# Kernel tuning notes

Hardware: AMD Instinct MI355X
Metric: run time of the kernel (lower is better)

## Reference

```python
import jax, jax.numpy as jnp
import numpy as np

N = 100000   # nodes
E = 1600000  # edges


def setup_inputs() -> dict:
    key = jax.random.key(0)
    ks = jax.random.split(key, 9)
    return {
        "in_feat": jax.random.normal(ks[0], (N, 256), jnp.float32),
        "W": jax.random.normal(ks[1], (256, 128), jnp.float32) * 0.05,
        "attn_l": jax.random.normal(ks[2], (1, 128), jnp.float32) * 0.1,
        "attn_r": jax.random.normal(ks[3], (1, 128), jnp.float32) * 0.1,
        "bias": jax.random.normal(ks[4], (1, 128), jnp.float32) * 0.01,
        "fc_w": jax.random.normal(ks[5], (128, 2), jnp.float32) * 0.1,
        "fc_b": jax.random.normal(ks[6], (2,), jnp.float32) * 0.01,
        "src": jax.random.randint(ks[7], (E,), 0, N, jnp.int32),
        "dst": jax.random.randint(ks[8], (E,), 0, N, jnp.int32),
    }


def reference(in_feat, W, attn_l, attn_r, bias, fc_w, fc_b, src, dst):
    # GATConv, num_heads=1 (head dim kept implicit since it is squeezed anyway)
    h = in_feat @ W                              # [N, F] projected features
    el = jnp.sum(h * attn_l, axis=-1)            # [N] left attention logits
    er = jnp.sum(h * attn_r, axis=-1)            # [N] right attention logits
    e = jax.nn.leaky_relu(el[src] + er[dst], negative_slope=0.2)  # [E]
    # edge softmax segmented by destination node (numerically stable)
    m = jax.ops.segment_max(e, dst, num_segments=N)               # [N]
    ex = jnp.exp(e - m[dst])                                      # [E]
    s = jax.ops.segment_sum(ex, dst, num_segments=N)              # [N]
    alpha = ex / jnp.where(s == 0, 1.0, s)[dst]                   # [E]
    # attention-weighted aggregation of source features to destinations
    agg = jax.ops.segment_sum(alpha[:, None] * h[src], dst, num_segments=N)  # [N, F]
    agg = agg + bias                                              # GATConv bias
    # head: ReLU -> Linear -> sigmoid
    out = jax.nn.sigmoid(jax.nn.relu(agg) @ fc_w + fc_b)          # [N, C]
    return out
```

## Files before the change

### kernel.cpp

```cpp
#include <hip/hip_runtime.h>
#include <cstdint>
#include <cstddef>

#define N_NODES 100000
#define E_EDGES 1600000
#define F_IN 256
#define F_OUT 128
#define NBKT 391
#define OBCAP 5120
#define GEMM_NB 1563
#define WCVT_NB 128

#define GLOBAL_AS __attribute__((address_space(1)))
#define LDS_AS    __attribute__((address_space(3)))

typedef __attribute__((ext_vector_type(8))) short  short8v;
typedef __attribute__((ext_vector_type(4))) float  float4v;

__device__ __forceinline__ unsigned short f2bf(float x) {
    union { float f; unsigned u; } v; v.f = x;
    unsigned r = v.u + 0x7fffu + ((v.u >> 16) & 1u);
    return (unsigned short)(r >> 16);
}

__device__ __forceinline__ unsigned cvt_pk_bf16(float lo, float hi) {
    unsigned r;
    asm("v_cvt_pk_bf16_f32 %0, %1, %2" : "=v"(r) : "v"(lo), "v"(hi));
    return r;
}

__global__ __launch_bounds__(256) void wcvt_hist(const float* __restrict__ W,
                                                 unsigned short* __restrict__ Wt,
                                                 const int* __restrict__ dst,
                                                 int* __restrict__ bcnt) {
    __shared__ int h[NBKT];
    int t = threadIdx.x;
    if (blockIdx.x < WCVT_NB) {
        int i = blockIdx.x * 256 + t;
        int k = i >> 7, j = i & 127;
        Wt[j * F_IN + k] = f2bf(W[i]);
        return;
    }
    int b = blockIdx.x - WCVT_NB;
    for (int i = t; i < NBKT; i += 256) h[i] = 0;
    __syncthreads();
    int e0  = b * 4096;
    int end = min(e0 + 4096, E_EDGES);
    for (int i = e0 + t; i < end; i += 256) atomicAdd(&h[dst[i] >> 8], 1);
    __syncthreads();
    for (int i = t; i < NBKT; i += 256) if (h[i]) atomicAdd(&bcnt[i], h[i]);
}

__global__ __launch_bounds__(512) void k_scan(const int* __restrict__ bcnt,
                                              int* __restrict__ bbase,
                                              int* __restrict__ bcur) {
    __shared__ int s[512];
    int t = threadIdx.x;
    int d = (t < NBKT) ? bcnt[t] : 0;
    s[t] = d;
    __syncthreads();
    for (int off = 1; off < 512; off <<= 1) {
        int v = (t >= off) ? s[t - off] : 0;
        __syncthreads();
        s[t] += v;
        __syncthreads();
    }
    if (t < NBKT) { int ex = s[t] - d; bbase[t] = ex; bcur[t] = ex; }
    if (t == NBKT - 1) bbase[NBKT] = s[t];
}

__global__ __launch_bounds__(256) void gemm_scatter(const float* __restrict__ A,
                                                    const unsigned short* __restrict__ Wt,
                                                    const float* __restrict__ attn_l,
                                                    const float* __restrict__ attn_r,
                                                    unsigned short* __restrict__ Hb,
                                                    float* __restrict__ el,
                                                    float* __restrict__ er,
                                                    const int* __restrict__ src,
                                                    const int* __restrict__ dst,
                                                    int* __restrict__ bcur,
                                                    unsigned int* __restrict__ epack) {
    __shared__ char smem[32 * 1024];
    int tid = threadIdx.x;

    if (blockIdx.x >= GEMM_NB) {
        int* h = (int*)smem;
        int b = blockIdx.x - GEMM_NB;
        for (int i = tid; i < NBKT; i += 256) h[i] = 0;
        __syncthreads();
        int e0  = b * 4096;
        int end = min(e0 + 4096, E_EDGES);
        #pragma unroll
        for (int j = 0; j < 16; ++j) {
            int i = e0 + j * 256 + tid;
            if (i < end) atomicAdd(&h[dst[i] >> 8], 1);
        }
        __syncthreads();
        for (int i = tid; i < NBKT; i += 256) {
            int c = h[i];
            h[i] = c ? atomicAdd(&bcur[i], c) : 0;
        }
        __syncthreads();
        #pragma unroll
        for (int j = 0; j < 16; ++j) {
            int i = e0 + j * 256 + tid;
            if (i < end) {
                int dv = dst[i];
                int p = atomicAdd(&h[dv >> 8], 1);
                epack[p] = (unsigned)src[i] | ((unsigned)(dv & 255) << 17);
            }
        }
        return;
    }

    float*          Afs = (float*)smem;
    unsigned short* Bs  = (unsigned short*)(smem + 16 * 1024);
    int wave = tid >> 6, lane = tid & 63;
    int g = lane >> 4, c = lane & 15;
    int row0 = blockIdx.x * 64;
    float4v acc[8] = {};

    int a_r[4], a_k[4], a_w[4];
    #pragma unroll
    for (int i = 0; i < 4; ++i) {
        int W_ = i * 1024 + tid * 4;
        int r  = W_ >> 6;
        a_w[i] = W_;
        a_r[i] = min(row0 + r, N_NODES - 1);
        a_k[i] = (W_ & 63) ^ ((r & 15) << 2);
    }
    int b_j[4], b_k[4], b_u[4];
    #pragma unroll
    for (int i = 0; i < 4; ++i) {
        int U_ = i * 2048 + tid * 8;
        int j  = U_ >> 6;
        b_u[i] = U_;
        b_j[i] = j;
        b_k[i] = (U_ & 63) ^ ((j & 7) << 3);
    }

    for (int k0 = 0; k0 < F_IN; k0 += 64) {
        #pragma unroll
        for (int i = 0; i < 4; ++i) {
            __builtin_amdgcn_global_load_lds(
                (const GLOBAL_AS unsigned int*)(A + (size_t)a_r[i] * F_IN + k0 + a_k[i]),
                (LDS_AS unsigned int*)&Afs[a_w[i]], 16, 0, 0);
        }
        #pragma unroll
        for (int i = 0; i < 4; ++i) {
            __builtin_amdgcn_global_load_lds(
                (const GLOBAL_AS unsigned int*)(Wt + (size_t)b_j[i] * F_IN + k0 + b_k[i]),
                (LDS_AS unsigned int*)&Bs[b_u[i]], 16, 0, 0);
        }
        __syncthreads();
        int arow = wave * 16 + c;
        int aswz = (arow & 15) << 2;
        #pragma unroll
        for (int ks = 0; ks < 2; ++ks) {
            int woff = arow * 64 + ks * 32 + g * 8;
            float4 a0 = *reinterpret_cast<float4*>(&Afs[(woff)     ^ aswz]);
            float4 a1 = *reinterpret_cast<float4*>(&Afs[(woff + 4) ^ aswz]);
            unsigned u[4];
            u[0] = cvt_pk_bf16(a0.x, a0.y);
            u[1] = cvt_pk_bf16(a0.z, a0.w);
            u[2] = cvt_pk_bf16(a1.x, a1.y);
            u[3] = cvt_pk_bf16(a1.z, a1.w);
            short8v af = *reinterpret_cast<short8v*>(u);
            #pragma unroll
            for (int nt = 0; nt < 8; ++nt) {
                int j = nt * 16 + c;
                int boff = (j * 64 + ks * 32 + g * 8) ^ ((j & 7) << 3);
                short8v bf = *reinterpret_cast<short8v*>(&Bs[boff]);
                acc[nt] = __builtin_amdgcn_mfma_f32_16x16x32_bf16(af, bf, acc[nt], 0, 0, 0);
            }
        }
        __syncthreads();
    }

    float al[8], ar[8];
    #pragma unroll
    for (int nt = 0; nt < 8; ++nt) {
        al[nt] = attn_l[nt * 16 + c];
        ar[nt] = attn_r[nt * 16 + c];
    }
    #pragma unroll
    for (int r = 0; r < 4; ++r) {
        int grow = row0 + wave * 16 + g * 4 + r;
        float sl = 0.f, sr = 0.f;
        #pragma unroll
        for (int nt = 0; nt < 8; ++nt) {
            float h = acc[nt][r];
            sl += h * al[nt];
            sr += h * ar[nt];
        }
        if (grow < N_NODES) {
            #pragma unroll
            for (int nt = 0; nt < 8; ++nt)
                Hb[(size_t)grow * F_OUT + nt * 16 + c] = f2bf(acc[nt][r]);
        }
        #pragma unroll
        for (int off = 1; off < 16; off <<= 1) {
            sl += __shfl_xor(sl, off);
            sr += __shfl_xor(sr, off);
        }
        if (c == 0 && grow < N_NODES) { el[grow] = sl; er[grow] = sr; }
    }
}

__global__ __launch_bounds__(256) void k_sort2(const unsigned int* __restrict__ epack,
                                               const int* __restrict__ bbase,
                                               const float* __restrict__ el,
                                               const float* __restrict__ er,
                                               float2* __restrict__ exs,
                                               int* __restrict__ rowptr,
                                               int* __restrict__ deg) {
    __shared__ int hist[256], cur[256], s[256];
    __shared__ float ssl[256];
    __shared__ unsigned obuf[OBCAP];
    __shared__ float exb[OBCAP];
    int b = blockIdx.x, t = threadIdx.x;
    int base = bbase[b], end = bbase[b + 1];
    int cnt  = end - base;
    hist[t] = 0;
    ssl[t] = 0.f;
    __syncthreads();
    for (int i = t; i < cnt; i += 256) atomicAdd(&hist[epack[base + i] >> 17], 1);
    __syncthreads();
    int d = hist[t];
    s[t] = d;
    __syncthreads();
    for (int off = 1; off < 256; off <<= 1) {
        int v = (t >= off) ? s[t - off] : 0;
        __syncthreads();
        s[t] += v;
        __syncthreads();
    }
    int excl = s[t] - d;
    int n = b * 256 + t;
    if (n < N_NODES) { deg[n] = d; rowptr[n] = base + excl; }
    cur[t] = excl;
    __syncthreads();
    for (int i = t; i < cnt; i += 256) {
        unsigned e = epack[base + i];
        int d2  = e >> 17;
        int sid = (int)(e & 0x1FFFFu);
        float tv = el[sid] + er[b * 256 + d2];
        tv = tv > 0.f ? tv : 0.2f * tv;
        float ex = __expf(tv);
        int p = atomicAdd(&cur[d2], 1);
        if (p < OBCAP) { obuf[p] = e; exb[p] = ex; }
        atomicAdd(&ssl[d2], ex);
    }
    __syncthreads();
    for (int i = t; i < cnt; i += 256) {
        unsigned e = obuf[i];
        float alpha = exb[i] / ssl[e >> 17];
        exs[base + i] = make_float2(alpha, __uint_as_float((e & 0x1FFFFu) << 8));
    }
}

__global__ __launch_bounds__(256) void agg_fused(const int* __restrict__ rowptr,
                                                 const int* __restrict__ deg,
                                                 const float2* __restrict__ exs,
                                                 const char* __restrict__ Hc,
                                                 const float* __restrict__ bias,
                                                 const float* __restrict__ fcw,
                                                 const float* __restrict__ fcb,
                                                 float* __restrict__ out) {
    __shared__ float2 exbuf[4][64];
    int tid   = threadIdx.x;
    int wslot = tid >> 6;
    int wid   = (blockIdx.x * 256 + tid) >> 6;
    int lane  = tid & 63;
    if (wid >= N_NODES) return;
    int grp = lane >> 4, fl = lane & 15;
    int start = rowptr[wid];
    int dg    = deg[wid];
    float acc[8] = {};
    float2* eb = exbuf[wslot];
    unsigned flb = (unsigned)fl << 4;

    for (int base = 0; base < dg; base += 64) {
        int cnt = min(64, dg - base);
        float2 p2 = make_float2(0.f, 0.f);
        if (lane < cnt) p2 = exs[start + base + lane];
        eb[lane] = p2;
        __builtin_amdgcn_wave_barrier();
        int nq = (cnt + 3) >> 2;
        #pragma unroll 2
        for (int q = 0; q < nq; ++q) {
            float2 p = eb[q * 4 + grp];
            float aq = p.x;
            uint4 v = *(const uint4*)(Hc + (__float_as_uint(p.y) + flb));
            acc[0] += aq * __uint_as_float(v.x << 16);
            acc[1] += aq * __uint_as_float(v.x & 0xffff0000u);
            acc[2] += aq * __uint_as_float(v.y << 16);
            acc[3] += aq * __uint_as_float(v.y & 0xffff0000u);
            acc[4] += aq * __uint_as_float(v.z << 16);
            acc[5] += aq * __uint_as_float(v.z & 0xffff0000u);
            acc[6] += aq * __uint_as_float(v.w << 16);
            acc[7] += aq * __uint_as_float(v.w & 0xffff0000u);
        }
        __builtin_amdgcn_wave_barrier();
    }

    #pragma unroll
    for (int j = 0; j < 8; ++j) {
        acc[j] += __shfl_xor(acc[j], 16);
        acc[j] += __shfl_xor(acc[j], 32);
    }

    float4 b0 = ((const float4*)bias)[fl * 2];
    float4 b1 = ((const float4*)bias)[fl * 2 + 1];
    float d0 = 0.f, d1 = 0.f;
    #pragma unroll
    for (int j = 0; j < 8; ++j) {
        float bj = j < 4 ? (&b0.x)[j] : (&b1.x)[j - 4];
        float vv = fmaxf(acc[j] + bj, 0.f);
        float2 wj = ((const float2*)fcw)[fl * 8 + j];
        d0 += vv * wj.x;
        d1 += vv * wj.y;
    }
    #pragma unroll
    for (int off = 1; off < 16; off <<= 1) {
        d0 += __shfl_xor(d0, off);
        d1 += __shfl_xor(d1, off);
    }
    if (lane == 0) {
        out[(size_t)wid * 2 + 0] = 1.f / (1.f + __expf(-(d0 + fcb[0])));
        out[(size_t)wid * 2 + 1] = 1.f / (1.f + __expf(-(d1 + fcb[1])));
    }
}

extern "C" void kernel_launch(void* const* d_in, const int* in_sizes, int n_in,
                              void* d_out, int out_size, void* d_ws, size_t ws_size,
                              hipStream_t stream) {
    const float* in_feat = (const float*)d_in[0];
    const float* W       = (const float*)d_in[1];
    const float* attn_l  = (const float*)d_in[2];
    const float* attn_r  = (const float*)d_in[3];
    const float* bias    = (const float*)d_in[4];
    const float* fc_w    = (const float*)d_in[5];
    const float* fc_b    = (const float*)d_in[6];
    const int*   src     = (const int*)d_in[7];
    const int*   dst     = (const int*)d_in[8];
    float* out = (float*)d_out;

    char* p = (char*)d_ws;
    unsigned short* HB = (unsigned short*)p; p += (size_t)N_NODES * F_OUT * sizeof(unsigned short);
    unsigned short* WT = (unsigned short*)p; p += (size_t)F_IN * F_OUT * sizeof(unsigned short);
    float* EL     = (float*)p; p += (size_t)N_NODES * sizeof(float);
    float* ER     = (float*)p; p += (size_t)N_NODES * sizeof(float);
    int*   DEG    = (int*)p;   p += (size_t)N_NODES * sizeof(int);
    int*   ROWPTR = (int*)p;   p += (size_t)N_NODES * sizeof(int);
    int*   BCNT   = (int*)p;   p += 512 * sizeof(int);
    int*   BBASE  = (int*)p;   p += 512 * sizeof(int);
    int*   BCUR   = (int*)p;   p += 512 * sizeof(int);
    unsigned int* EPACK = (unsigned int*)p; p += (size_t)E_EDGES * sizeof(unsigned int);
    float2* EXS   = (float2*)p; p += (size_t)E_EDGES * sizeof(float2);

    hipMemsetAsync(BCNT, 0, 512 * sizeof(int), stream);

    wcvt_hist<<<WCVT_NB + NBKT, 256, 0, stream>>>(W, WT, dst, BCNT);
    k_scan   <<<1, 512, 0, stream>>>(BCNT, BBASE, BCUR);
    gemm_scatter<<<GEMM_NB + NBKT, 256, 0, stream>>>(
        in_feat, WT, attn_l, attn_r, HB, EL, ER, src, dst, BCUR, EPACK);
    k_sort2  <<<NBKT, 256, 0, stream>>>(EPACK, BBASE, EL, ER, EXS, ROWPTR, DEG);

    agg_fused<<<(N_NODES * 64 + 255) / 256, 256, 0, stream>>>(
        ROWPTR, DEG, EXS, (const char*)HB, bias, fc_w, fc_b, out);
}
```

Before: 149.5 us.

## Store per-block bucket histograms and precompute scatter offsets in a parallel scan

The histogram kernel now writes each edge-chunk's per-bucket counts to a global table. A new multi-block scan turns that table into exact per-chunk, per-bucket write offsets. The scatter blocks in the GEMM kernel then load those offsets directly instead of recounting destinations and taking global atomics on shared bucket cursors. This removes a second pass over dst and the atomic contention, at the cost of an extra table and a 391-block scan launch with column-strided accesses.

```diff
diff --git a/kernel.cpp b/kernel.cpp
--- a/kernel.cpp
+++ b/kernel.cpp
@@ -10,6 +10,7 @@
 #define OBCAP 5120
 #define GEMM_NB 1563
 #define WCVT_NB 128
+#define HSTR 400
 
 #define GLOBAL_AS __attribute__((address_space(1)))
 #define LDS_AS    __attribute__((address_space(3)))
@@ -32,7 +33,8 @@
 __global__ __launch_bounds__(256) void wcvt_hist(const float* __restrict__ W,
                                                  unsigned short* __restrict__ Wt,
                                                  const int* __restrict__ dst,
-                                                 int* __restrict__ bcnt) {
+                                                 int* __restrict__ bcnt,
+                                                 int* __restrict__ hist) {
     __shared__ int h[NBKT];
     int t = threadIdx.x;
     if (blockIdx.x < WCVT_NB) {
@@ -48,14 +50,20 @@
     int end = min(e0 + 4096, E_EDGES);
     for (int i = e0 + t; i < end; i += 256) atomicAdd(&h[dst[i] >> 8], 1);
     __syncthreads();
-    for (int i = t; i < NBKT; i += 256) if (h[i]) atomicAdd(&bcnt[i], h[i]);
-}
-
-__global__ __launch_bounds__(512) void k_scan(const int* __restrict__ bcnt,
-                                              int* __restrict__ bbase,
-                                              int* __restrict__ bcur) {
+    for (int i = t; i < NBKT; i += 256) {
+        int c = h[i];
+        hist[b * HSTR + i] = c;
+        if (c) atomicAdd(&bcnt[i], c);
+    }
+}
+
+__global__ __launch_bounds__(512) void k_scan2(const int* __restrict__ bcnt,
+                                               int* __restrict__ bbase,
+                                               int* __restrict__ hist) {
     __shared__ int s[512];
+    __shared__ int base_sh;
     int t = threadIdx.x;
+    int i = blockIdx.x;
     int d = (t < NBKT) ? bcnt[t] : 0;
     s[t] = d;
     __syncthreads();
@@ -65,8 +73,25 @@
         s[t] += v;
         __syncthreads();
     }
-    if (t < NBKT) { int ex = s[t] - d; bbase[t] = ex; bcur[t] = ex; }
-    if (t == NBKT - 1) bbase[NBKT] = s[t];
+    if (t == 0) {
+        int bi = (i > 0) ? s[i - 1] : 0;
+        base_sh = bi;
+        bbase[i] = bi;
+        if (i == NBKT - 1) bbase[NBKT] = s[NBKT - 1];
+    }
+    __syncthreads();
+    int base_i = base_sh;
+    int hv = (t < NBKT) ? hist[t * HSTR + i] : 0;
+    __syncthreads();
+    s[t] = hv;
+    __syncthreads();
+    for (int off = 1; off < 512; off <<= 1) {
+        int v = (t >= off) ? s[t - off] : 0;
+        __syncthreads();
+        s[t] += v;
+        __syncthreads();
+    }
+    if (t < NBKT) hist[t * HSTR + i] = s[t] - hv + base_i;
 }
 
 __global__ __launch_bounds__(256) void gemm_scatter(const float* __restrict__ A,
@@ -78,7 +103,7 @@
                                                     float* __restrict__ er,
                                                     const int* __restrict__ src,
                                                     const int* __restrict__ dst,
-                                                    int* __restrict__ bcur,
+                                                    const int* __restrict__ hist,
                                                     unsigned int* __restrict__ epack) {
     __shared__ char smem[32 * 1024];
     int tid = threadIdx.x;
@@ -86,21 +111,10 @@
     if (blockIdx.x >= GEMM_NB) {
         int* h = (int*)smem;
         int b = blockIdx.x - GEMM_NB;
-        for (int i = tid; i < NBKT; i += 256) h[i] = 0;
+        for (int i = tid; i < NBKT; i += 256) h[i] = hist[b * HSTR + i];
         __syncthreads();
         int e0  = b * 4096;
         int end = min(e0 + 4096, E_EDGES);
-        #pragma unroll
-        for (int j = 0; j < 16; ++j) {
-            int i = e0 + j * 256 + tid;
-            if (i < end) atomicAdd(&h[dst[i] >> 8], 1);
-        }
-        __syncthreads();
-        for (int i = tid; i < NBKT; i += 256) {
-            int c = h[i];
-            h[i] = c ? atomicAdd(&bcur[i], c) : 0;
-        }
-        __syncthreads();
         #pragma unroll
         for (int j = 0; j < 16; ++j) {
             int i = e0 + j * 256 + tid;
@@ -355,16 +369,16 @@
     int*   ROWPTR = (int*)p;   p += (size_t)N_NODES * sizeof(int);
     int*   BCNT   = (int*)p;   p += 512 * sizeof(int);
     int*   BBASE  = (int*)p;   p += 512 * sizeof(int);
-    int*   BCUR   = (int*)p;   p += 512 * sizeof(int);
+    int*   HIST   = (int*)p;   p += (size_t)NBKT * HSTR * sizeof(int);
     unsigned int* EPACK = (unsigned int*)p; p += (size_t)E_EDGES * sizeof(unsigned int);
     float2* EXS   = (float2*)p; p += (size_t)E_EDGES * sizeof(float2);
 
     hipMemsetAsync(BCNT, 0, 512 * sizeof(int), stream);
 
-    wcvt_hist<<<WCVT_NB + NBKT, 256, 0, stream>>>(W, WT, dst, BCNT);
-    k_scan   <<<1, 512, 0, stream>>>(BCNT, BBASE, BCUR);
+    wcvt_hist<<<WCVT_NB + NBKT, 256, 0, stream>>>(W, WT, dst, BCNT, HIST);
+    k_scan2  <<<NBKT, 512, 0, stream>>>(BCNT, BBASE, HIST);
     gemm_scatter<<<GEMM_NB + NBKT, 256, 0, stream>>>(
-        in_feat, WT, attn_l, attn_r, HB, EL, ER, src, dst, BCUR, EPACK);
+        in_feat, WT, attn_l, attn_r, HB, EL, ER, src, dst, HIST, EPACK);
     k_sort2  <<<NBKT, 256, 0, stream>>>(EPACK, BBASE, EL, ER, EXS, ROWPTR, DEG);
 
     agg_fused<<<(N_NODES * 64 + 255) / 256, 256, 0, stream>>>(
```

Result: faster. 145.9 us, median of 3 (-2.4%).
